# Kernel tuning notes

Hardware: AMD Instinct MI355X
Metric: run time of the kernel (lower is better)

## Reference

```python
import jax, jax.numpy as jnp
import numpy as np

N_USER, N_MERCH, N_EDGE, D, H = 200000, 50000, 2000000, 64, 64


def _segment_mean(vals, idx, num_segments):
    # vals: [E, D] gathered source features; idx: [E] destination ids
    s = jax.ops.segment_sum(vals, idx, num_segments=num_segments)
    c = jax.ops.segment_sum(jnp.ones((idx.shape[0], 1), vals.dtype), idx,
                            num_segments=num_segments)
    return s / jnp.maximum(c, 1.0)


def _hetero_sage(x_u, x_m, bases, coeff, root, b, u_idx, m_idx):
    # basis-decomposed per-edge-type message weights (to_hetero_with_bases)
    W_pays = jnp.einsum('b,bij->ij', coeff[0], bases)  # user -> merchant
    W_rev = jnp.einsum('b,bij->ij', coeff[1], bases)   # merchant -> user
    # SAGEConv: aggregate-then-transform (mean aggregation)
    agg_m = _segment_mean(x_u[u_idx], m_idx, x_m.shape[0])
    agg_u = _segment_mean(x_m[m_idx], u_idx, x_u.shape[0])
    h_m = agg_m @ W_pays + x_m @ root + b
    h_u = agg_u @ W_rev + x_u @ root + b
    return h_u, h_m


def setup_inputs() -> dict:
    key = jax.random.key(0)
    ks = jax.random.split(key, 12)
    sD = 1.0 / np.sqrt(D)
    sH = 1.0 / np.sqrt(H)
    inp = {
        'x_user': jax.random.normal(ks[0], (N_USER, D), jnp.float32),
        'x_merch': jax.random.normal(ks[1], (N_MERCH, D), jnp.float32),
        'bases1': jax.random.normal(ks[2], (3, D, H), jnp.float32) * sD,
        'coeff1': jax.random.normal(ks[3], (2, 3), jnp.float32),
        'root1': jax.random.normal(ks[4], (D, H), jnp.float32) * sD,
        'b1': jnp.zeros((H,), jnp.float32),
        'bases2': jax.random.normal(ks[5], (3, H, H), jnp.float32) * sH,
        'coeff2': jax.random.normal(ks[6], (2, 3), jnp.float32),
        'root2': jax.random.normal(ks[7], (H, H), jnp.float32) * sH,
        'b2': jnp.zeros((H,), jnp.float32),
        'w_mlp1': jax.random.normal(ks[8], (2 * H, H), jnp.float32) / np.sqrt(2 * H),
        'b_mlp1': jnp.zeros((H,), jnp.float32),
        'w_mlp2': jax.random.normal(ks[9], (H, 2), jnp.float32) * sH,
        'b_mlp2': jnp.zeros((2,), jnp.float32),
    }
    u_idx = jax.random.randint(ks[10], (N_EDGE,), 0, N_USER, jnp.int64 if jax.config.jax_enable_x64 else jnp.int32)
    m_idx = jax.random.randint(ks[11], (N_EDGE,), 0, N_MERCH, u_idx.dtype)
    inp['edge_index'] = jnp.stack([u_idx, m_idx])  # [2, E]
    return inp


def reference(x_user, x_merch, bases1, coeff1, root1, b1,
              bases2, coeff2, root2, b2,
              w_mlp1, b_mlp1, w_mlp2, b_mlp2, edge_index):
    u_idx, m_idx = edge_index[0], edge_index[1]
    h_u, h_m = _hetero_sage(x_user, x_merch, bases1, coeff1, root1, b1, u_idx, m_idx)
    h_u, h_m = jax.nn.relu(h_u), jax.nn.relu(h_m)
    h_u, h_m = _hetero_sage(h_u, h_m, bases2, coeff2, root2, b2, u_idx, m_idx)
    # edge classifier: gather-concat-MLP
    z = jnp.concatenate([h_u[u_idx], h_m[m_idx]], axis=1)  # [E, 2H]
    logits = jax.nn.relu(z @ w_mlp1 + b_mlp1) @ w_mlp2 + b_mlp2  # [E, 2]
    return logits
```

## Files before the change

### kernel.cpp

```cpp
#include <hip/hip_runtime.h>


typedef __attribute__((ext_vector_type(8))) short short8;
typedef __attribute__((ext_vector_type(4))) float f32x4;

__device__ inline unsigned short f2bf(float f) {
  unsigned u = __float_as_uint(f);
  u += 0x7FFF + ((u >> 16) & 1);
  return (unsigned short)(u >> 16);
}
__device__ inline float bf2f(unsigned short h) {
  return __uint_as_float(((unsigned)h) << 16);
}
__device__ inline float bf2fs(short h) { return bf2f((unsigned short)h); }

__global__ __launch_bounds__(256) void sort_hist_mkW1(
    const int* __restrict__ u_idx, const int* __restrict__ m_idx,
    int* __restrict__ hist_u, int* __restrict__ hist_m, int E, int nblk,
    const float* __restrict__ bases1, const float* __restrict__ coeff1,
    const float* __restrict__ root1,
    const float* __restrict__ bases2, const float* __restrict__ coeff2,
    float* __restrict__ Wcat1u, float* __restrict__ Wcat1m,
    float* __restrict__ wp2, float* __restrict__ wr2) {
  int t = threadIdx.x, blk = blockIdx.x;
  if (blk >= nblk) {
    int ij = (blk - nblk) * 256 + t;
    float a0 = bases1[ij], a1 = bases1[4096 + ij], a2 = bases1[8192 + ij];
    Wcat1m[ij] = coeff1[0] * a0 + coeff1[1] * a1 + coeff1[2] * a2;
    Wcat1u[ij] = coeff1[3] * a0 + coeff1[4] * a1 + coeff1[5] * a2;
    float r = root1[ij];
    Wcat1m[4096 + ij] = r;
    Wcat1u[4096 + ij] = r;
    float c0 = bases2[ij], c1 = bases2[4096 + ij], c2 = bases2[8192 + ij];
    wp2[ij] = coeff2[0] * c0 + coeff2[1] * c1 + coeff2[2] * c2;
    wr2[ij] = coeff2[3] * c0 + coeff2[4] * c1 + coeff2[5] * c2;
    return;
  }
  __shared__ int hu[256], hm[256];
  hu[t] = 0; hm[t] = 0;
  __syncthreads();
  int e0 = blk * 2048 + t;
#pragma unroll
  for (int i = 0; i < 8; ++i) {
    int e = e0 + i * 256;
    if (e < E) {
      atomicAdd(&hu[u_idx[e] >> 10], 1);
      atomicAdd(&hm[m_idx[e] >> 8], 1);
    }
  }
  __syncthreads();
  hist_u[t * nblk + blk] = hu[t];
  hist_m[t * nblk + blk] = hm[t];
}

__global__ __launch_bounds__(256) void scanA2_mkW2(
    int* __restrict__ hist_u, int* __restrict__ hist_m,
    int* __restrict__ part, int nhist, int sb,
    const float* __restrict__ wp2, const float* __restrict__ wr2,
    const float* __restrict__ root2, const float* __restrict__ w_mlp1,
    const float* __restrict__ b2, const float* __restrict__ b_mlp1,
    float* __restrict__ Wcat2u, float* __restrict__ Wcat2m,
    float* __restrict__ bu2, float* __restrict__ bm2) {
  int blk = blockIdx.x;
  if (blk >= 2 * sb) {
    int tid = (blk - 2 * sb) * 256 + threadIdx.x;
    int i = tid >> 6, j = tid & 63;
    float au = 0.f, ru = 0.f, am = 0.f, rm = 0.f;
    for (int k = 0; k < 64; ++k) {
      float wa = w_mlp1[k * 64 + j];
      float wb = w_mlp1[(64 + k) * 64 + j];
      au += wr2[i * 64 + k] * wa;
      ru += root2[i * 64 + k] * wa;
      am += wp2[i * 64 + k] * wb;
      rm += root2[i * 64 + k] * wb;
    }
    Wcat2u[tid] = au; Wcat2u[4096 + tid] = ru;
    Wcat2m[tid] = am; Wcat2m[4096 + tid] = rm;
    if (i == 0) {
      float s1 = 0.f, s2 = 0.f;
      for (int k = 0; k < 64; ++k) {
        s1 += b2[k] * w_mlp1[k * 64 + j];
        s2 += b2[k] * w_mlp1[(64 + k) * 64 + j];
      }
      bu2[j] = s1;
      bm2[j] = s2 + b_mlp1[j];
    }
    return;
  }
  int* arr; int* prt;
  if (blk < sb) { arr = hist_u; prt = part; }
  else { arr = hist_m; prt = part + 256; blk -= sb; }
  __shared__ int s[256];
  int t = threadIdx.x;
  int base = blk * 2048 + t * 8;
  int v[8]; int sum = 0;
#pragma unroll
  for (int i = 0; i < 8; ++i) { int idx = base + i; v[i] = (idx < nhist) ? arr[idx] : 0; sum += v[i]; }
  s[t] = sum;
  __syncthreads();
  for (int ofs = 1; ofs < 256; ofs <<= 1) {
    int a = (t >= ofs) ? s[t - ofs] : 0;
    __syncthreads();
    s[t] += a;
    __syncthreads();
  }
  int run = s[t] - sum;
#pragma unroll
  for (int i = 0; i < 8; ++i) { int idx = base + i; if (idx < nhist) arr[idx] = run; run += v[i]; }
  if (t == 255) prt[blk] = s[255];
}

__global__ __launch_bounds__(256) void scanB2_packW4(
    int* __restrict__ part, int NB,
    const float* __restrict__ s0, const float* __restrict__ s1,
    const float* __restrict__ s2, const float* __restrict__ s3,
    unsigned short* __restrict__ d0, unsigned short* __restrict__ d1,
    unsigned short* __restrict__ d2, unsigned short* __restrict__ d3) {
  int blk = blockIdx.x;
  if (blk >= 2) {
    int gid = (blk - 2) * 256 + threadIdx.x;
    int mat = gid >> 13;
    int tid = gid & 8191;
    int frag = tid >> 9;
    int nt = frag >> 2, ks = frag & 3;
    int lane = (tid >> 3) & 63;
    int i = tid & 7;
    int k = ks * 32 + (lane >> 4) * 8 + i;
    int col = nt * 16 + (lane & 15);
    const float* s = (mat == 0) ? s0 : (mat == 1) ? s1 : (mat == 2) ? s2 : s3;
    unsigned short* d = (mat == 0) ? d0 : (mat == 1) ? d1 : (mat == 2) ? d2 : d3;
    d[tid] = f2bf(s[k * 64 + col]);
    return;
  }
  int* prt = part + blk * 256;
  __shared__ int s[256];
  int t = threadIdx.x;
  int v = (t < NB) ? prt[t] : 0;
  s[t] = v;
  __syncthreads();
  for (int ofs = 1; ofs < 256; ofs <<= 1) {
    int a = (t >= ofs) ? s[t - ofs] : 0;
    __syncthreads();
    s[t] += a;
    __syncthreads();
  }
  if (t < NB) prt[t] = s[t] - v;
}

__global__ __launch_bounds__(256) void sort_scatter1_tobf16(
    const int* __restrict__ u_idx, const int* __restrict__ m_idx,
    const int* __restrict__ hist_u, const int* __restrict__ hist_m,
    const int* __restrict__ part,
    unsigned* __restrict__ stage_u, unsigned* __restrict__ stage_m,
    int E, int nblk,
    const float* __restrict__ xu, unsigned short* __restrict__ xbu, int n4u,
    const float* __restrict__ xm, unsigned short* __restrict__ xbm, int n4m) {
  int t = threadIdx.x, blk = blockIdx.x;
  if (blk >= nblk) {
    int i = (blk - nblk) * 256 + t;
    int stride = 512 * 256;
    int tot = n4u + n4m;
    for (int j = i; j < tot; j += stride) {
      float4 v = (j < n4u) ? reinterpret_cast<const float4*>(xu)[j]
                           : reinterpret_cast<const float4*>(xm)[j - n4u];
      ushort4 o;
      o.x = f2bf(v.x); o.y = f2bf(v.y); o.z = f2bf(v.z); o.w = f2bf(v.w);
      if (j < n4u) reinterpret_cast<ushort4*>(xbu)[j] = o;
      else reinterpret_cast<ushort4*>(xbm)[j - n4u] = o;
    }
    return;
  }
  __shared__ int cu[256], cm[256];
  int idx = t * nblk + blk;
  cu[t] = hist_u[idx] + part[idx >> 11];
  cm[t] = hist_m[idx] + part[256 + (idx >> 11)];
  __syncthreads();
  int e0 = blk * 2048 + t;
#pragma unroll
  for (int i = 0; i < 8; ++i) {
    int e = e0 + i * 256;
    if (e < E) {
      int u = u_idx[e], m = m_idx[e];
      int pu = atomicAdd(&cu[u >> 10], 1);
      stage_u[pu] = ((unsigned)(u & 1023) << 16) | (unsigned)m;
      int pm = atomicAdd(&cm[m >> 8], 1);
      stage_m[pm] = ((unsigned)(m & 255) << 18) | (unsigned)u;
    }
  }
}

template <int LOWBITS, int SHIFT, typename VT>
__device__ __forceinline__ void bucket_body(
    const unsigned* __restrict__ stage, const int* __restrict__ hs,
    const int* __restrict__ prt,
    VT* __restrict__ vals_out, int* __restrict__ off,
    int E, int N, int nblk, int b) {
  constexpr int NBIN = 1 << LOWBITS;
  constexpr int R = NBIN / 256;
  constexpr unsigned VMASK = (1u << SHIFT) - 1u;
  __shared__ int h[NBIN];
  __shared__ int s[256];
  int t = threadIdx.x;
  int i0 = b * nblk;
  int seg0 = hs[i0] + prt[i0 >> 11];
  int seg1 = E;
  if (b != 255) { int i1 = (b + 1) * nblk; seg1 = hs[i1] + prt[i1 >> 11]; }
#pragma unroll
  for (int r = 0; r < R; ++r) h[t * R + r] = 0;
  __syncthreads();
  for (int i = seg0 + t; i < seg1; i += 256)
    atomicAdd(&h[stage[i] >> SHIFT], 1);
  __syncthreads();
  int vals[R]; int loc = 0;
#pragma unroll
  for (int r = 0; r < R; ++r) { vals[r] = h[t * R + r]; loc += vals[r]; }
  s[t] = loc;
  __syncthreads();
  for (int ofs = 1; ofs < 256; ofs <<= 1) {
    int a = (t >= ofs) ? s[t - ofs] : 0;
    __syncthreads();
    s[t] += a;
    __syncthreads();
  }
  int run = seg0 + s[t] - loc;
#pragma unroll
  for (int r = 0; r < R; ++r) {
    int bin = t * R + r;
    h[bin] = run;
    int node = (b << LOWBITS) + bin;
    if (node <= N) off[node] = run;
    run += vals[r];
  }
  __syncthreads();
  for (int i = seg0 + t; i < seg1; i += 256) {
    unsigned v = stage[i];
    int pos = atomicAdd(&h[v >> SHIFT], 1);
    vals_out[pos] = (VT)(v & VMASK);
  }
}

__global__ __launch_bounds__(256) void sort_bucket2(
    const unsigned* __restrict__ stage_u, const int* __restrict__ hist_u,
    unsigned short* __restrict__ csr_u, int* __restrict__ off_u, int Nu,
    const unsigned* __restrict__ stage_m, const int* __restrict__ hist_m,
    int* __restrict__ csr_m, int* __restrict__ off_m, int Nm,
    const int* __restrict__ part, int E, int nblk) {
  if (blockIdx.x < 256)
    bucket_body<10, 16, unsigned short>(stage_u, hist_u, part, csr_u, off_u,
                                        E, Nu, nblk, blockIdx.x);
  else
    bucket_body<8, 18, int>(stage_m, hist_m, part + 256, csr_m, off_m,
                            E, Nm, nblk, blockIdx.x - 256);
}

template <typename IT, int RELU>
__device__ __forceinline__ void agg_body(
    unsigned short (*A)[16][128],
    const unsigned short* __restrict__ src,
    const unsigned short* __restrict__ selfF,
    const int* __restrict__ off, const IT* __restrict__ csr,
    const unsigned short* __restrict__ Wp,
    const float* __restrict__ bias,
    unsigned short* __restrict__ out, int N, int blk) {
  int t = threadIdx.x, wave = t >> 6, lane = t & 63;
  int nbase = (blk * 4 + wave) * 16;
  if (nbase >= N) return;
  int fl = lane & 7, sub = lane >> 3;
  const short8* src8 = (const short8*)src;
  char* rowbase = (char*)&A[wave][0][0];
#pragma unroll 1
  for (int j = 0; j < 2; ++j) {
    int g = sub * 2 + j;
    int n = nbase + g;
    float ac[8] = {0.f, 0.f, 0.f, 0.f, 0.f, 0.f, 0.f, 0.f};
    float inv = 1.f;
    short8 sf8 = {0, 0, 0, 0, 0, 0, 0, 0};
    if (n < N) {
      int beg = off[n], end = off[n + 1], k = beg;
      for (; k + 4 <= end; k += 4) {
        int s0 = (int)csr[k], s1 = (int)csr[k + 1];
        int s2 = (int)csr[k + 2], s3 = (int)csr[k + 3];
        short8 r0 = src8[(size_t)s0 * 8 + fl];
        short8 r1 = src8[(size_t)s1 * 8 + fl];
        short8 r2 = src8[(size_t)s2 * 8 + fl];
        short8 r3 = src8[(size_t)s3 * 8 + fl];
#pragma unroll
        for (int c = 0; c < 8; ++c)
          ac[c] += (bf2fs(r0[c]) + bf2fs(r1[c])) + (bf2fs(r2[c]) + bf2fs(r3[c]));
      }
      for (; k < end; ++k) {
        short8 r = src8[(size_t)((int)csr[k]) * 8 + fl];
#pragma unroll
        for (int c = 0; c < 8; ++c) ac[c] += bf2fs(r[c]);
      }
      inv = 1.f / fmaxf((float)(end - beg), 1.f);
      sf8 = ((const short8*)selfF)[(size_t)n * 8 + fl];
    }
    short8 ab;
#pragma unroll
    for (int c = 0; c < 8; ++c) ab[c] = (short)f2bf(ac[c] * inv);
    int swz = (g & 7) << 4;
    char* rp = rowbase + g * 256;
    *(short8*)(rp + ((fl * 16) ^ swz)) = ab;
    *(short8*)(rp + ((128 + fl * 16) ^ swz)) = sf8;
  }
  int r = lane & 15, q = lane >> 4;
  int swzr = (r & 7) << 4;
  const char* arow = rowbase + r * 256;
  short8 af[4];
#pragma unroll
  for (int ks = 0; ks < 4; ++ks)
    af[ks] = *(const short8*)(arow + ((ks * 64 + q * 16) ^ swzr));
  const short8* wp8 = (const short8*)Wp;
#pragma unroll
  for (int nt = 0; nt < 4; ++nt) {
    float b = bias[nt * 16 + r];
    f32x4 acc = {b, b, b, b};
#pragma unroll
    for (int ks = 0; ks < 4; ++ks) {
      short8 bf = wp8[(nt * 4 + ks) * 64 + lane];
      acc = __builtin_amdgcn_mfma_f32_16x16x32_bf16(af[ks], bf, acc, 0, 0, 0);
    }
#pragma unroll
    for (int j = 0; j < 4; ++j) {
      int n = nbase + q * 4 + j;
      if (n < N) {
        float v = acc[j];
        if (RELU) v = fmaxf(v, 0.f);
        out[(size_t)n * 64 + nt * 16 + r] = f2bf(v);
      }
    }
  }
}

template <int RELU>
__global__ __launch_bounds__(256) void agg_dual(
    const unsigned short* __restrict__ srcA, const unsigned short* __restrict__ selfA,
    const int* __restrict__ offA, const int* __restrict__ csrA,
    const unsigned short* __restrict__ WpA, const float* __restrict__ biasA,
    unsigned short* __restrict__ outA, int NA, int gbA,
    const unsigned short* __restrict__ srcB, const unsigned short* __restrict__ selfB,
    const int* __restrict__ offB, const unsigned short* __restrict__ csrB,
    const unsigned short* __restrict__ WpB, const float* __restrict__ biasB,
    unsigned short* __restrict__ outB, int NB) {
  __shared__ unsigned short A[4][16][128];
  int blk = blockIdx.x;
  if (blk < gbA)
    agg_body<int, RELU>(A, srcA, selfA, offA, csrA, WpA, biasA, outA, NA, blk);
  else
    agg_body<unsigned short, RELU>(A, srcB, selfB, offB, csrB, WpB, biasB, outB, NB, blk - gbA);
}

__global__ __launch_bounds__(256) void edge_mlp(
    const unsigned short* __restrict__ pu, const unsigned short* __restrict__ pm,
    const int* __restrict__ u_idx, const int* __restrict__ m_idx,
    const float* __restrict__ w2, const float* __restrict__ bvec,
    float* __restrict__ out, int E) {
  int t = threadIdx.x;
  int lane = t & 63;
  int sub = lane >> 4;
  int fl = lane & 15;
  int f = fl * 4;
  int wid = (blockIdx.x * 256 + t) >> 6;
  int nw = (gridDim.x * 256) >> 6;
  float4 wA = reinterpret_cast<const float4*>(w2)[2 * fl];
  float4 wB = reinterpret_cast<const float4*>(w2)[2 * fl + 1];
  float ob0 = bvec[0], ob1 = bvec[1];
  int ngrp = (E + 7) >> 3;
  for (int g = wid; g < ngrp; g += nw) {
    int eA = g * 8 + sub, eB = eA + 4;
    bool vA = eA < E, vB = eB < E;
    int exA = vA ? eA : 0, exB = vB ? eB : 0;
    int uA = __builtin_nontemporal_load(&u_idx[exA]);
    int mA = __builtin_nontemporal_load(&m_idx[exA]);
    int uB = __builtin_nontemporal_load(&u_idx[exB]);
    int mB = __builtin_nontemporal_load(&m_idx[exB]);
    ushort4 a4A = *reinterpret_cast<const ushort4*>(&pu[(size_t)uA * 64 + f]);
    ushort4 b4A = *reinterpret_cast<const ushort4*>(&pm[(size_t)mA * 64 + f]);
    ushort4 a4B = *reinterpret_cast<const ushort4*>(&pu[(size_t)uB * 64 + f]);
    ushort4 b4B = *reinterpret_cast<const ushort4*>(&pm[(size_t)mB * 64 + f]);
    float v0 = fmaxf(bf2f(a4A.x) + bf2f(b4A.x), 0.f);
    float v1 = fmaxf(bf2f(a4A.y) + bf2f(b4A.y), 0.f);
    float v2 = fmaxf(bf2f(a4A.z) + bf2f(b4A.z), 0.f);
    float v3 = fmaxf(bf2f(a4A.w) + bf2f(b4A.w), 0.f);
    float p0 = v0 * wA.x + v1 * wA.z + v2 * wB.x + v3 * wB.z;
    float p1 = v0 * wA.y + v1 * wA.w + v2 * wB.y + v3 * wB.w;
    float w0 = fmaxf(bf2f(a4B.x) + bf2f(b4B.x), 0.f);
    float w1 = fmaxf(bf2f(a4B.y) + bf2f(b4B.y), 0.f);
    float w2v = fmaxf(bf2f(a4B.z) + bf2f(b4B.z), 0.f);
    float w3 = fmaxf(bf2f(a4B.w) + bf2f(b4B.w), 0.f);
    float q0 = w0 * wA.x + w1 * wA.z + w2v * wB.x + w3 * wB.z;
    float q1 = w0 * wA.y + w1 * wA.w + w2v * wB.y + w3 * wB.w;
#pragma unroll
    for (int o = 8; o; o >>= 1) {
      p0 += __shfl_xor(p0, o); p1 += __shfl_xor(p1, o);
      q0 += __shfl_xor(q0, o); q1 += __shfl_xor(q1, o);
    }
    if (fl == 0) {
      if (vA) *reinterpret_cast<float2*>(&out[(size_t)eA * 2]) = make_float2(p0 + ob0, p1 + ob1);
      if (vB) *reinterpret_cast<float2*>(&out[(size_t)eB * 2]) = make_float2(q0 + ob0, q1 + ob1);
    }
  }
}

extern "C" void kernel_launch(void* const* d_in, const int* in_sizes, int n_in,
                              void* d_out, int out_size, void* d_ws, size_t ws_size,
                              hipStream_t stream) {
  const float* x_user  = (const float*)d_in[0];
  const float* x_merch = (const float*)d_in[1];
  const float* bases1  = (const float*)d_in[2];
  const float* coeff1  = (const float*)d_in[3];
  const float* root1   = (const float*)d_in[4];
  const float* b1      = (const float*)d_in[5];
  const float* bases2  = (const float*)d_in[6];
  const float* coeff2  = (const float*)d_in[7];
  const float* root2   = (const float*)d_in[8];
  const float* b2      = (const float*)d_in[9];
  const float* w_mlp1  = (const float*)d_in[10];
  const float* b_mlp1  = (const float*)d_in[11];
  const float* w_mlp2  = (const float*)d_in[12];
  const float* b_mlp2  = (const float*)d_in[13];
  const int*   edge_ix = (const int*)d_in[14];

  const int Nu = in_sizes[0] / 64;
  const int Nm = in_sizes[1] / 64;
  const int E  = in_sizes[14] / 2;
  const int* u_idx = edge_ix;
  const int* m_idx = edge_ix + E;

  char* p = (char*)d_ws;
  auto alloc = [&](size_t bytes) -> char* {
    char* r = p;
    p += (bytes + 255) & ~(size_t)255;
    return r;
  };
  int* off_u = (int*)alloc((size_t)(Nu + 1) * 4);
  int* off_m = (int*)alloc((size_t)(Nm + 1) * 4);
  int* part  = (int*)alloc(512 * 4);
  unsigned short* csr_u = (unsigned short*)alloc((size_t)E * 2);
  int* csr_m = (int*)alloc((size_t)E * 4);
  unsigned short* xb_u = (unsigned short*)alloc((size_t)Nu * 64 * 2);
  unsigned short* xb_m = (unsigned short*)alloc((size_t)Nm * 64 * 2);
  unsigned short* h_u  = (unsigned short*)alloc((size_t)Nu * 64 * 2);
  unsigned short* h_m  = (unsigned short*)alloc((size_t)Nm * 64 * 2);
  float* Wcat1u = (float*)alloc(8192 * 4);
  float* Wcat1m = (float*)alloc(8192 * 4);
  float* Wcat2u = (float*)alloc(8192 * 4);
  float* Wcat2m = (float*)alloc(8192 * 4);
  unsigned short* Wp1u = (unsigned short*)alloc(8192 * 2);
  unsigned short* Wp1m = (unsigned short*)alloc(8192 * 2);
  unsigned short* Wp2u = (unsigned short*)alloc(8192 * 2);
  unsigned short* Wp2m = (unsigned short*)alloc(8192 * 2);
  float* wp2 = (float*)alloc(4096 * 4);
  float* wr2 = (float*)alloc(4096 * 4);
  float* bu2 = (float*)alloc(64 * 4);
  float* bm2 = (float*)alloc(64 * 4);
  if ((size_t)(p - (char*)d_ws) > ws_size) return;

  const int nblk = (E + 2047) / 2048;
  const int nhist = 256 * nblk;
  const int sb = (nhist + 2047) / 2048;
  unsigned* stage_u = (unsigned*)h_u;
  unsigned* stage_m = stage_u + E;
  int* hist_u = (int*)h_m;
  int* hist_m = hist_u + nhist;

  sort_hist_mkW1<<<nblk + 16, 256, 0, stream>>>(
      u_idx, m_idx, hist_u, hist_m, E, nblk,
      bases1, coeff1, root1, bases2, coeff2, Wcat1u, Wcat1m, wp2, wr2);
  scanA2_mkW2<<<2 * sb + 16, 256, 0, stream>>>(
      hist_u, hist_m, part, nhist, sb,
      wp2, wr2, root2, w_mlp1, b2, b_mlp1, Wcat2u, Wcat2m, bu2, bm2);
  scanB2_packW4<<<130, 256, 0, stream>>>(
      part, sb, Wcat1u, Wcat1m, Wcat2u, Wcat2m, Wp1u, Wp1m, Wp2u, Wp2m);
  sort_scatter1_tobf16<<<nblk + 512, 256, 0, stream>>>(
      u_idx, m_idx, hist_u, hist_m, part, stage_u, stage_m, E, nblk,
      x_user, xb_u, Nu * 16, x_merch, xb_m, Nm * 16);
  sort_bucket2<<<512, 256, 0, stream>>>(stage_u, hist_u, csr_u, off_u, Nu,
                                        stage_m, hist_m, csr_m, off_m, Nm,
                                        part, E, nblk);

  int gbu = (Nu + 63) / 64, gbm = (Nm + 63) / 64;
  agg_dual<1><<<gbm + gbu, 256, 0, stream>>>(
      xb_u, xb_m, off_m, csr_m, Wp1m, b1, h_m, Nm, gbm,
      xb_m, xb_u, off_u, csr_u, Wp1u, b1, h_u, Nu);
  unsigned short* pm_buf = xb_m;
  unsigned short* pu_buf = xb_u;
  agg_dual<0><<<gbm + gbu, 256, 0, stream>>>(
      h_u, h_m, off_m, csr_m, Wp2m, bm2, pm_buf, Nm, gbm,
      h_m, h_u, off_u, csr_u, Wp2u, bu2, pu_buf, Nu);

  edge_mlp<<<2048, 256, 0, stream>>>(pu_buf, pm_buf, u_idx, m_idx,
                                     w_mlp2, b_mlp2, (float*)d_out, E);
}
```

Measured before the change: 341.5 us.

## Vectorize index loads, move bf16 conversion earlier, tune agg unroll, nontemporal output

Moves the feature fp32-to-bf16 conversion blocks from the scatter kernel into the histogram kernel, so they overlap with histogramming. The histogram and scatter passes now load 8 contiguous indices per thread with int4 loads instead of strided scalar loads. The aggregation loop gets a template unroll factor, 8 for merchant nodes with higher degree and 4 for users. Edge logits are written with nontemporal stores. Register pressure from the wider unroll may reduce occupancy.

```diff
diff --git a/kernel.cpp b/kernel.cpp
--- a/kernel.cpp
+++ b/kernel.cpp
@@ -3,6 +3,7 @@
 
 typedef __attribute__((ext_vector_type(8))) short short8;
 typedef __attribute__((ext_vector_type(4))) float f32x4;
+typedef __attribute__((ext_vector_type(2))) float f32x2;
 
 __device__ inline unsigned short f2bf(float f) {
   unsigned u = __float_as_uint(f);
@@ -14,15 +15,31 @@
 }
 __device__ inline float bf2fs(short h) { return bf2f((unsigned short)h); }
 
-__global__ __launch_bounds__(256) void sort_hist_mkW1(
+__global__ __launch_bounds__(256) void sort_hist_mkW1_tobf16(
     const int* __restrict__ u_idx, const int* __restrict__ m_idx,
     int* __restrict__ hist_u, int* __restrict__ hist_m, int E, int nblk,
     const float* __restrict__ bases1, const float* __restrict__ coeff1,
     const float* __restrict__ root1,
     const float* __restrict__ bases2, const float* __restrict__ coeff2,
     float* __restrict__ Wcat1u, float* __restrict__ Wcat1m,
-    float* __restrict__ wp2, float* __restrict__ wr2) {
+    float* __restrict__ wp2, float* __restrict__ wr2,
+    const float* __restrict__ xu, unsigned short* __restrict__ xbu, int n4u,
+    const float* __restrict__ xm, unsigned short* __restrict__ xbm, int n4m) {
   int t = threadIdx.x, blk = blockIdx.x;
+  if (blk >= nblk + 16) {
+    int i = (blk - nblk - 16) * 256 + t;
+    int stride = 512 * 256;
+    int tot = n4u + n4m;
+    for (int j = i; j < tot; j += stride) {
+      float4 v = (j < n4u) ? reinterpret_cast<const float4*>(xu)[j]
+                           : reinterpret_cast<const float4*>(xm)[j - n4u];
+      ushort4 o;
+      o.x = f2bf(v.x); o.y = f2bf(v.y); o.z = f2bf(v.z); o.w = f2bf(v.w);
+      if (j < n4u) reinterpret_cast<ushort4*>(xbu)[j] = o;
+      else reinterpret_cast<ushort4*>(xbm)[j - n4u] = o;
+    }
+    return;
+  }
   if (blk >= nblk) {
     int ij = (blk - nblk) * 256 + t;
     float a0 = bases1[ij], a1 = bases1[4096 + ij], a2 = bases1[8192 + ij];
@@ -39,11 +56,22 @@
   __shared__ int hu[256], hm[256];
   hu[t] = 0; hm[t] = 0;
   __syncthreads();
-  int e0 = blk * 2048 + t;
-#pragma unroll
-  for (int i = 0; i < 8; ++i) {
-    int e = e0 + i * 256;
-    if (e < E) {
+  int base = blk * 2048 + t * 8;
+  if (base + 8 <= E) {
+    int4 ua = *reinterpret_cast<const int4*>(u_idx + base);
+    int4 ub = *reinterpret_cast<const int4*>(u_idx + base + 4);
+    int4 ma = *reinterpret_cast<const int4*>(m_idx + base);
+    int4 mb = *reinterpret_cast<const int4*>(m_idx + base + 4);
+    atomicAdd(&hu[ua.x >> 10], 1); atomicAdd(&hu[ua.y >> 10], 1);
+    atomicAdd(&hu[ua.z >> 10], 1); atomicAdd(&hu[ua.w >> 10], 1);
+    atomicAdd(&hu[ub.x >> 10], 1); atomicAdd(&hu[ub.y >> 10], 1);
+    atomicAdd(&hu[ub.z >> 10], 1); atomicAdd(&hu[ub.w >> 10], 1);
+    atomicAdd(&hm[ma.x >> 8], 1); atomicAdd(&hm[ma.y >> 8], 1);
+    atomicAdd(&hm[ma.z >> 8], 1); atomicAdd(&hm[ma.w >> 8], 1);
+    atomicAdd(&hm[mb.x >> 8], 1); atomicAdd(&hm[mb.y >> 8], 1);
+    atomicAdd(&hm[mb.z >> 8], 1); atomicAdd(&hm[mb.w >> 8], 1);
+  } else {
+    for (int e = base; e < E; ++e) {
       atomicAdd(&hu[u_idx[e] >> 10], 1);
       atomicAdd(&hm[m_idx[e] >> 8], 1);
     }
@@ -147,39 +175,36 @@
   if (t < NB) prt[t] = s[t] - v;
 }
 
-__global__ __launch_bounds__(256) void sort_scatter1_tobf16(
+__global__ __launch_bounds__(256) void sort_scatter1(
     const int* __restrict__ u_idx, const int* __restrict__ m_idx,
     const int* __restrict__ hist_u, const int* __restrict__ hist_m,
     const int* __restrict__ part,
     unsigned* __restrict__ stage_u, unsigned* __restrict__ stage_m,
-    int E, int nblk,
-    const float* __restrict__ xu, unsigned short* __restrict__ xbu, int n4u,
-    const float* __restrict__ xm, unsigned short* __restrict__ xbm, int n4m) {
+    int E, int nblk) {
+  __shared__ int cu[256], cm[256];
   int t = threadIdx.x, blk = blockIdx.x;
-  if (blk >= nblk) {
-    int i = (blk - nblk) * 256 + t;
-    int stride = 512 * 256;
-    int tot = n4u + n4m;
-    for (int j = i; j < tot; j += stride) {
-      float4 v = (j < n4u) ? reinterpret_cast<const float4*>(xu)[j]
-                           : reinterpret_cast<const float4*>(xm)[j - n4u];
-      ushort4 o;
-      o.x = f2bf(v.x); o.y = f2bf(v.y); o.z = f2bf(v.z); o.w = f2bf(v.w);
-      if (j < n4u) reinterpret_cast<ushort4*>(xbu)[j] = o;
-      else reinterpret_cast<ushort4*>(xbm)[j - n4u] = o;
-    }
-    return;
-  }
-  __shared__ int cu[256], cm[256];
   int idx = t * nblk + blk;
   cu[t] = hist_u[idx] + part[idx >> 11];
   cm[t] = hist_m[idx] + part[256 + (idx >> 11)];
   __syncthreads();
-  int e0 = blk * 2048 + t;
-#pragma unroll
-  for (int i = 0; i < 8; ++i) {
-    int e = e0 + i * 256;
-    if (e < E) {
+  int base = blk * 2048 + t * 8;
+  if (base + 8 <= E) {
+    int4 ua = *reinterpret_cast<const int4*>(u_idx + base);
+    int4 ub = *reinterpret_cast<const int4*>(u_idx + base + 4);
+    int4 ma = *reinterpret_cast<const int4*>(m_idx + base);
+    int4 mb = *reinterpret_cast<const int4*>(m_idx + base + 4);
+    int us[8] = {ua.x, ua.y, ua.z, ua.w, ub.x, ub.y, ub.z, ub.w};
+    int ms[8] = {ma.x, ma.y, ma.z, ma.w, mb.x, mb.y, mb.z, mb.w};
+#pragma unroll
+    for (int i = 0; i < 8; ++i) {
+      int u = us[i], m = ms[i];
+      int pu = atomicAdd(&cu[u >> 10], 1);
+      stage_u[pu] = ((unsigned)(u & 1023) << 16) | (unsigned)m;
+      int pm = atomicAdd(&cm[m >> 8], 1);
+      stage_m[pm] = ((unsigned)(m & 255) << 18) | (unsigned)u;
+    }
+  } else {
+    for (int e = base; e < E; ++e) {
       int u = u_idx[e], m = m_idx[e];
       int pu = atomicAdd(&cu[u >> 10], 1);
       stage_u[pu] = ((unsigned)(u & 1023) << 16) | (unsigned)m;
@@ -253,7 +278,7 @@
                             E, Nm, nblk, blockIdx.x - 256);
 }
 
-template <typename IT, int RELU>
+template <typename IT, int RELU, int U>
 __device__ __forceinline__ void agg_body(
     unsigned short (*A)[16][128],
     const unsigned short* __restrict__ src,
@@ -277,16 +302,15 @@
     short8 sf8 = {0, 0, 0, 0, 0, 0, 0, 0};
     if (n < N) {
       int beg = off[n], end = off[n + 1], k = beg;
-      for (; k + 4 <= end; k += 4) {
-        int s0 = (int)csr[k], s1 = (int)csr[k + 1];
-        int s2 = (int)csr[k + 2], s3 = (int)csr[k + 3];
-        short8 r0 = src8[(size_t)s0 * 8 + fl];
-        short8 r1 = src8[(size_t)s1 * 8 + fl];
-        short8 r2 = src8[(size_t)s2 * 8 + fl];
-        short8 r3 = src8[(size_t)s3 * 8 + fl];
-#pragma unroll
-        for (int c = 0; c < 8; ++c)
-          ac[c] += (bf2fs(r0[c]) + bf2fs(r1[c])) + (bf2fs(r2[c]) + bf2fs(r3[c]));
+      for (; k + U <= end; k += U) {
+        short8 r[U];
+#pragma unroll
+        for (int x = 0; x < U; ++x)
+          r[x] = src8[(size_t)((int)csr[k + x]) * 8 + fl];
+#pragma unroll
+        for (int x = 0; x < U; ++x)
+#pragma unroll
+          for (int c = 0; c < 8; ++c) ac[c] += bf2fs(r[x][c]);
       }
       for (; k < end; ++k) {
         short8 r = src8[(size_t)((int)csr[k]) * 8 + fl];
@@ -346,9 +370,9 @@
   __shared__ unsigned short A[4][16][128];
   int blk = blockIdx.x;
   if (blk < gbA)
-    agg_body<int, RELU>(A, srcA, selfA, offA, csrA, WpA, biasA, outA, NA, blk);
+    agg_body<int, RELU, 8>(A, srcA, selfA, offA, csrA, WpA, biasA, outA, NA, blk);
   else
-    agg_body<unsigned short, RELU>(A, srcB, selfB, offB, csrB, WpB, biasB, outB, NB, blk - gbA);
+    agg_body<unsigned short, RELU, 4>(A, srcB, selfB, offB, csrB, WpB, biasB, outB, NB, blk - gbA);
 }
 
 __global__ __launch_bounds__(256) void edge_mlp(
@@ -397,8 +421,14 @@
       q0 += __shfl_xor(q0, o); q1 += __shfl_xor(q1, o);
     }
     if (fl == 0) {
-      if (vA) *reinterpret_cast<float2*>(&out[(size_t)eA * 2]) = make_float2(p0 + ob0, p1 + ob1);
-      if (vB) *reinterpret_cast<float2*>(&out[(size_t)eB * 2]) = make_float2(q0 + ob0, q1 + ob1);
+      if (vA) {
+        f32x2 oA = {p0 + ob0, p1 + ob1};
+        __builtin_nontemporal_store(oA, (f32x2*)&out[(size_t)eA * 2]);
+      }
+      if (vB) {
+        f32x2 oB = {q0 + ob0, q1 + ob1};
+        __builtin_nontemporal_store(oB, (f32x2*)&out[(size_t)eB * 2]);
+      }
     }
   }
 }
@@ -465,17 +495,17 @@
   int* hist_u = (int*)h_m;
   int* hist_m = hist_u + nhist;
 
-  sort_hist_mkW1<<<nblk + 16, 256, 0, stream>>>(
+  sort_hist_mkW1_tobf16<<<nblk + 16 + 512, 256, 0, stream>>>(
       u_idx, m_idx, hist_u, hist_m, E, nblk,
-      bases1, coeff1, root1, bases2, coeff2, Wcat1u, Wcat1m, wp2, wr2);
+      bases1, coeff1, root1, bases2, coeff2, Wcat1u, Wcat1m, wp2, wr2,
+      x_user, xb_u, Nu * 16, x_merch, xb_m, Nm * 16);
   scanA2_mkW2<<<2 * sb + 16, 256, 0, stream>>>(
       hist_u, hist_m, part, nhist, sb,
       wp2, wr2, root2, w_mlp1, b2, b_mlp1, Wcat2u, Wcat2m, bu2, bm2);
   scanB2_packW4<<<130, 256, 0, stream>>>(
       part, sb, Wcat1u, Wcat1m, Wcat2u, Wcat2m, Wp1u, Wp1m, Wp2u, Wp2m);
-  sort_scatter1_tobf16<<<nblk + 512, 256, 0, stream>>>(
-      u_idx, m_idx, hist_u, hist_m, part, stage_u, stage_m, E, nblk,
-      x_user, xb_u, Nu * 16, x_merch, xb_m, Nm * 16);
+  sort_scatter1<<<nblk, 256, 0, stream>>>(
+      u_idx, m_idx, hist_u, hist_m, part, stage_u, stage_m, E, nblk);
   sort_bucket2<<<512, 256, 0, stream>>>(stage_u, hist_u, csr_u, off_u, Nu,
                                         stage_m, hist_m, csr_m, off_m, Nm,
                                         part, E, nblk);
```

After: 344.4 us. About the same (+0.8%).
